# Performance work log

Hardware: AMD Instinct MI355X
Metric: run time of the kernel (lower is better)

Reference implementation:

```python
import jax, jax.numpy as jnp
import numpy as np

N = 50000   # nodes
E = 800000  # edges (avg degree 16)
D = 128     # node feature dim
DE = 16     # edge feature dim
H = 128     # MLP hidden dim
MSG_IN = 2 * D + DE + 1  # src feat + dst feat + edge feat + squared distance


def setup_inputs() -> dict:
    key = jax.random.key(0)
    ks = jax.random.split(key, 10)
    def wmat(k, shp):
        return jax.random.normal(k, shp, jnp.float32) * 0.05
    return {
        "f": jax.random.normal(ks[0], (N, D), jnp.float32),
        "x": jax.random.normal(ks[1], (N, 3), jnp.float32),
        "w": jax.random.normal(ks[2], (E, DE), jnp.float32),
        "src": jax.random.randint(ks[3], (E,), 0, N),
        "dst": jax.random.randint(ks[4], (E,), 0, N),
        "Wm1": wmat(ks[5], (MSG_IN, H)), "bm1": jnp.zeros((H,), jnp.float32),
        "Wm2": wmat(ks[6], (H, D)),      "bm2": jnp.zeros((D,), jnp.float32),
        "Wu1": wmat(ks[7], (D, H)),      "bu1": jnp.zeros((H,), jnp.float32),
        "Wu2": wmat(ks[8], (H, D)),      "bu2": jnp.zeros((D,), jnp.float32),
    }


def reference(f, x, w, src, dst, Wm1, bm1, Wm2, bm2, Wu1, bu1, Wu2, bu2):
    # message: gather endpoint features, squared distance, concat, MLP  [E, D]
    sqd = jnp.sum((x[src] - x[dst]) ** 2, axis=-1, keepdims=True)  # [E, 1]
    msg_in = jnp.concatenate([f[src], f[dst], w, sqd], axis=-1)    # [E, MSG_IN]
    m = jnp.dot(jax.nn.relu(jnp.dot(msg_in, Wm1) + bm1), Wm2) + bm2  # [E, D]
    # reduce: sum messages at destination nodes (DGL fn.sum)
    m_sum = jax.ops.segment_sum(m, dst, num_segments=N)             # [N, D]
    # update: node MLP on m_sum + f
    h = m_sum + f
    f_new = jnp.dot(jax.nn.relu(jnp.dot(h, Wu1) + bu1), Wu2) + bu2  # [N, D]
    return f_new
```

## Files before the change

kernel.cpp:

```cpp
#include <hip/hip_runtime.h>
#include <hip/hip_fp8.h>

#define D 128
#define HD 128
#define DE 16
#define MSG_IN 273
#define EB 64
#define NT 256
#define KP1 288
#define NCH2 4
#define NB 32
#define HID_PAD 132
#define CH8 (4 * EB * 64)
#define LDS1 (4 * EB * 64 + EB * 32)
#define OB 8192
#define OC 24576

typedef __attribute__((ext_vector_type(8))) short short8v;
typedef __attribute__((ext_vector_type(4))) float f32x4;
typedef unsigned short ushort_t;
typedef unsigned char uchar_t;

#define GLOAD_LDS16(gp, lp) \
    __builtin_amdgcn_global_load_lds((const __attribute__((address_space(1))) unsigned int*)(gp), \
                                     (__attribute__((address_space(3))) unsigned int*)(lp), 16, 0, 0)

__device__ __forceinline__ unsigned short f2bf(float v) {
    unsigned int u = __builtin_bit_cast(unsigned int, v);
    u += 0x7fffu + ((u >> 16) & 1u);
    return (unsigned short)(u >> 16);
}
__device__ __forceinline__ float bf2f(ushort_t u) {
    return __builtin_bit_cast(float, (unsigned int)u << 16);
}
__device__ __forceinline__ unsigned int cvt_pk_bf16(float lo, float hi) {
    unsigned int r;
    asm("v_cvt_pk_bf16_f32 %0, %1, %2" : "=v"(r) : "v"(lo), "v"(hi));
    return r;
}
__device__ __forceinline__ uchar_t f8e(float v) {
    __hip_fp8_e4m3 t(v);
    return (uchar_t)t.__x;
}
__device__ __forceinline__ float f8d(unsigned b) {
    unsigned t = ((b & 0x7fu) << 20) | ((b & 0x80u) << 24);
    return __builtin_bit_cast(float, t) * 0x1p120f;
}

__global__ void fused_pre_kernel(const float* __restrict__ Wm1, const float* __restrict__ Wm2,
                                 const float* __restrict__ Wu1, const float* __restrict__ Wu2,
                                 ushort_t* __restrict__ W1p, ushort_t* __restrict__ W2p,
                                 ushort_t* __restrict__ Wu1p, ushort_t* __restrict__ Wu2p,
                                 const float* __restrict__ f, ushort_t* __restrict__ fb,
                                 const float* __restrict__ w, ushort_t* __restrict__ wbf,
                                 const int* __restrict__ dst, int* __restrict__ cnt,
                                 int n8, int nw8, int E) {
    const int gid    = blockIdx.x * 256 + threadIdx.x;
    const int stride = gridDim.x * 256;
    const int rp1 = 128 * KP1;
    const int rp2 = rp1 + HD * D;
    const int rp_elems = rp2 + 2 * HD * D;
    for (int i = gid; i < rp_elems; i += stride) {
        if (i < rp1) {
            int n = i / KP1, k = i % KP1;
            W1p[i] = f2bf((k < MSG_IN) ? Wm1[(size_t)k * HD + n] : 0.f);
        } else if (i < rp2) {
            int i2 = i - rp1;
            int n = i2 / HD, k = i2 % HD;
            W2p[i2] = f2bf(Wm2[(size_t)k * D + n]);
        } else {
            int i2 = (i - rp2);
            const bool second = i2 >= HD * D;
            if (second) i2 -= HD * D;
            int n = i2 / HD, k = i2 % HD;
            if (second) Wu2p[i2] = f2bf(Wu2[(size_t)k * D + n]);
            else        Wu1p[i2] = f2bf(Wu1[(size_t)k * HD + n]);
        }
    }
    for (int i = gid; i < n8; i += stride) {
        float4 v0 = *(const float4*)(f + (size_t)i * 8);
        float4 v1 = *(const float4*)(f + (size_t)i * 8 + 4);
        union { ushort_t us[8]; short8v v; } pk;
        pk.us[0] = f2bf(v0.x); pk.us[1] = f2bf(v0.y);
        pk.us[2] = f2bf(v0.z); pk.us[3] = f2bf(v0.w);
        pk.us[4] = f2bf(v1.x); pk.us[5] = f2bf(v1.y);
        pk.us[6] = f2bf(v1.z); pk.us[7] = f2bf(v1.w);
        *(short8v*)(fb + (size_t)i * 8) = pk.v;
    }
    for (int i = gid; i < nw8; i += stride) {
        float4 v0 = *(const float4*)(w + (size_t)i * 8);
        float4 v1 = *(const float4*)(w + (size_t)i * 8 + 4);
        union { ushort_t us[8]; short8v v; } pk;
        pk.us[0] = f2bf(v0.x); pk.us[1] = f2bf(v0.y);
        pk.us[2] = f2bf(v0.z); pk.us[3] = f2bf(v0.w);
        pk.us[4] = f2bf(v1.x); pk.us[5] = f2bf(v1.y);
        pk.us[6] = f2bf(v1.z); pk.us[7] = f2bf(v1.w);
        *(short8v*)(wbf + (size_t)i * 8) = pk.v;
    }
    for (int i = gid; i < E; i += stride) atomicAdd(&cnt[dst[i]], 1);
}

__global__ __launch_bounds__(1024) void scan_kernel(const int* __restrict__ cnt,
                                                    int* __restrict__ roff,
                                                    int* __restrict__ cursor, int Nn) {
    __shared__ int wsum[16];
    const int t = threadIdx.x, l = t & 63, wid = t >> 6;
    int running = 0;
    for (int base = 0; base < Nn; base += 4096) {
        const int i0 = base + t * 4;
        int v0 = 0, v1 = 0, v2 = 0, v3 = 0;
        if (i0 + 3 < Nn) {
            int4 v = *(const int4*)(cnt + i0);
            v0 = v.x; v1 = v.y; v2 = v.z; v3 = v.w;
        } else {
            if (i0 + 0 < Nn) v0 = cnt[i0 + 0];
            if (i0 + 1 < Nn) v1 = cnt[i0 + 1];
            if (i0 + 2 < Nn) v2 = cnt[i0 + 2];
        }
        const int vsum = v0 + v1 + v2 + v3;
        int s = vsum;
        #pragma unroll
        for (int off = 1; off < 64; off <<= 1) {
            int u = __shfl_up(s, off, 64);
            if (l >= off) s += u;
        }
        if (l == 63) wsum[wid] = s;
        __syncthreads();
        if (wid == 0 && l < 16) {
            int xv = wsum[l];
            #pragma unroll
            for (int off = 1; off < 16; off <<= 1) {
                int u = __shfl_up(xv, off, 64);
                if (l >= off) xv += u;
            }
            wsum[l] = xv;
        }
        __syncthreads();
        const int prev  = (wid > 0) ? wsum[wid - 1] : 0;
        const int total = wsum[15];
        int ex = running + prev + (s - vsum);
        if (i0 + 0 < Nn) { roff[i0 + 0] = ex; cursor[i0 + 0] = ex; } ex += v0;
        if (i0 + 1 < Nn) { roff[i0 + 1] = ex; cursor[i0 + 1] = ex; } ex += v1;
        if (i0 + 2 < Nn) { roff[i0 + 2] = ex; cursor[i0 + 2] = ex; } ex += v2;
        if (i0 + 3 < Nn) { roff[i0 + 3] = ex; cursor[i0 + 3] = ex; }
        running += total;
        __syncthreads();
    }
}

__global__ void scatter_kernel(const int* __restrict__ dst, int* cursor,
                               const int* __restrict__ roff, const int* __restrict__ cnt,
                               int* __restrict__ perm, int* __restrict__ sdst,
                               float* __restrict__ mh, int E, int Nn) {
    const int gid    = blockIdx.x * 256 + threadIdx.x;
    const int stride = gridDim.x * 256;
    for (int i = gid; i < E; i += stride) {
        int d = dst[i];
        int s = atomicAdd(&cursor[d], 1);
        perm[s] = i;
        sdst[s] = d;
    }
    for (int n = gid; n < Nn; n += stride) {
        const int c = cnt[n];
        const int r = roff[n];
        const bool need0 = (c == 0) || (r / EB != (r + c - 1) / EB);
        if (need0) {
            float4 z = {0.f, 0.f, 0.f, 0.f};
            float* p = mh + (size_t)n * D;
            #pragma unroll
            for (int k = 0; k < 32; ++k) *(float4*)(p + k * 4) = z;
        }
    }
}

__global__ __launch_bounds__(NT, 4) void ab_kernel(
    const ushort_t* __restrict__ fbf,
    const ushort_t* __restrict__ W1p,
    uchar_t* __restrict__ Af, ushort_t* __restrict__ Bf16, int Nn)
{
    __shared__ __align__(16) ushort_t lds[2 * 64 * 64];

    const int t    = threadIdx.x;
    const int lane = t & 63;
    const int wv   = t >> 6;
    const int col  = lane & 15;
    const int g    = lane >> 4;
    const int n0   = blockIdx.x * 64;

    #pragma unroll
    for (int it = 0; it < 4; ++it) {
        const int gidx = it * 256 + t;
        const int row  = gidx >> 4;
        const int gr   = gidx & 15;
        const int pair = gr >> 3, s = gr & 7;
        const int sP   = s ^ (row & 7);
        const int gn   = min(n0 + row, Nn - 1);
        short8v v = *(const short8v*)(fbf + (size_t)gn * D + gr * 8);
        *(short8v*)&lds[(pair * 64 + row) * 64 + sP * 8] = v;
    }
    __syncthreads();

    const bool even = (col & 1) == 0;
    #pragma unroll
    for (int half = 0; half < 2; ++half) {
        f32x4 acc[4][2];
        #pragma unroll
        for (int rt = 0; rt < 4; ++rt) {
            acc[rt][0] = (f32x4){0.f, 0.f, 0.f, 0.f};
            acc[rt][1] = (f32x4){0.f, 0.f, 0.f, 0.f};
        }
        const int kbase = half * 128;
        #pragma unroll
        for (int c = 0; c < 4; ++c) {
            short8v b0 = *(const short8v*)&W1p[(size_t)(wv * 32 + col) * KP1 + kbase + c * 32 + g * 8];
            short8v b1 = *(const short8v*)&W1p[(size_t)(wv * 32 + 16 + col) * KP1 + kbase + c * 32 + g * 8];
            short8v a[4];
            #pragma unroll
            for (int rt = 0; rt < 4; ++rt) {
                const int row = rt * 16 + col;
                const int sP = (((c & 1) << 2) + g) ^ (row & 7);
                a[rt] = *(const short8v*)&lds[((c >> 1) * 64 + row) * 64 + sP * 8];
            }
            #pragma unroll
            for (int rt = 0; rt < 4; ++rt) {
                acc[rt][0] = __builtin_amdgcn_mfma_f32_16x16x32_bf16(a[rt], b0, acc[rt][0], 0, 0, 0);
                acc[rt][1] = __builtin_amdgcn_mfma_f32_16x16x32_bf16(a[rt], b1, acc[rt][1], 0, 0, 0);
            }
        }
        #pragma unroll
        for (int rt = 0; rt < 4; ++rt)
            #pragma unroll
            for (int j = 0; j < 2; ++j)
                #pragma unroll
                for (int r = 0; r < 4; ++r) {
                    const int row = rt * 16 + g * 4 + r;
                    const int gn = n0 + row;
                    float v  = acc[rt][j][r];
                    float vn = __shfl_xor(v, 1, 64);
                    if (even && gn < Nn) {
                        const int ca = wv * 32 + j * 16 + col;
                        if (half == 0) {
                            ushort_t pk = (ushort_t)f8e(v) | ((ushort_t)f8e(vn) << 8);
                            *(ushort_t*)(Af + (size_t)gn * D + ca) = pk;
                        } else {
                            *(unsigned int*)(Bf16 + (size_t)gn * D + ca) = cvt_pk_bf16(v, vn);
                        }
                    }
                }
    }
}

__global__ __launch_bounds__(NT, 4) void edge_lin_kernel(
    const uchar_t* __restrict__ Af, const ushort_t* __restrict__ Bf16,
    const float* __restrict__ x, const ushort_t* __restrict__ wbf,
    const int* __restrict__ src,
    const int* __restrict__ perm, const int* __restrict__ sdst,
    const ushort_t* __restrict__ W1p, const float* __restrict__ bm1,
    float* __restrict__ mh, int E)
{
    __shared__ __align__(16) uchar_t lds8[28672];
    __shared__ int s_rid[EB];
    __shared__ int s_dgs[EB];

    const int t    = threadIdx.x;
    const int lane = t & 63;
    const int wv   = t >> 6;
    const int e0   = blockIdx.x * EB;
    const int nvalid = min(EB, E - e0);

    const int myd  = (e0 + lane < E) ? sdst[e0 + lane] : -1;
    const int prevd = (e0 > 0) ? sdst[e0 - 1] : -2;
    const int nextd = (e0 + EB < E) ? sdst[e0 + EB] : -2;

    const int dprev_l = __shfl_up(myd, 1, 64);
    const bool head = (lane == 0) || (myd != dprev_l);
    const unsigned long long mask = __ballot(head && (lane < nvalid));
    const unsigned long long le = (lane == 63) ? ~0ull : ((1ull << (lane + 1)) - 1ull);
    const int rid = (int)__popcll(mask & le) - 1;
    const int ndist = (int)__popcll(mask);
    s_rid[lane] = (rid < 0) ? 0 : rid;
    if (head && lane < nvalid) s_dgs[rid] = myd;

    {
        const int el8 = lane >> 3;
        const int s   = lane & 7;
        const int sl  = s ^ el8;
        const int slA = min(e0 + wv * 16 + el8,     E - 1);
        const int slB = min(e0 + wv * 16 + 8 + el8, E - 1);
        const int nsA = src[perm[slA]];
        const int nsB = src[perm[slB]];
        GLOAD_LDS16(Af + (size_t)nsA * D + sl * 16, &lds8[(wv * 16    ) * 128]);
        GLOAD_LDS16(Af + (size_t)nsB * D + sl * 16, &lds8[(wv * 16 + 8) * 128]);
    }
    {
        const int ntask = ndist * 16;
        for (int idx = t; idx < ntask; idx += NT) {
            const int rowr = idx >> 4;
            const int gr   = idx & 15;
            const int dg   = s_dgs[rowr];
            uint4 v = *(const uint4*)(Bf16 + (size_t)dg * D + gr * 8);
            const int phys = gr ^ (rowr & 15);
            *(uint4*)&lds8[OB + rowr * 256 + phys * 16] = v;
        }
    }
    {
        const int el = lane >> 2, q = lane & 3;
        const int qp = q ^ (el & 3);
        const int slot = e0 + wv * 16 + el;
        const bool ok = slot < E;
        const int sc = min(slot, E - 1);
        const int ge = perm[sc];
        union { ushort_t us[8]; short8v v; } pk;
        #pragma unroll
        for (int j = 0; j < 8; ++j) pk.us[j] = 0;
        if (ok) {
            if (q < 2) {
                pk.v = *(const short8v*)(wbf + (size_t)ge * DE + q * 8);
            } else if (q == 2) {
                const int ns = src[ge], nd = sdst[sc];
                float dx = x[ns*3+0] - x[nd*3+0];
                float dy = x[ns*3+1] - x[nd*3+1];
                float dz = x[ns*3+2] - x[nd*3+2];
                pk.us[0] = f2bf(dx*dx + dy*dy + dz*dz);
            }
        }
        *(short8v*)&lds8[OC + (wv * 16 + el) * 64 + qp * 16] = pk.v;
    }

    const int col = lane & 15;
    const int g   = lane >> 4;

    short8v bc0 = *(const short8v*)&W1p[(size_t)(wv * 32 + col) * KP1 + 256 + g * 8];
    short8v bc1 = *(const short8v*)&W1p[(size_t)(wv * 32 + 16 + col) * KP1 + 256 + g * 8];

    __syncthreads();

    f32x4 acc[4][2];
    {
        float bv0 = bm1[wv * 32 + col];
        float bv1 = bm1[wv * 32 + 16 + col];
        #pragma unroll
        for (int rt = 0; rt < 4; ++rt) {
            acc[rt][0] = (f32x4){bv0, bv0, bv0, bv0};
            acc[rt][1] = (f32x4){bv1, bv1, bv1, bv1};
        }
    }
    #pragma unroll
    for (int rt = 0; rt < 4; ++rt) {
        const int row = rt * 16 + col;
        const int sP8 = g ^ (row & 3);
        short8v a = *(const short8v*)&lds8[OC + row * 64 + sP8 * 16];
        acc[rt][0] = __builtin_amdgcn_mfma_f32_16x16x32_bf16(a, bc0, acc[rt][0], 0, 0, 0);
        acc[rt][1] = __builtin_amdgcn_mfma_f32_16x16x32_bf16(a, bc1, acc[rt][1], 0, 0, 0);
    }

    float h[4][2][4];
    #pragma unroll
    for (int rt = 0; rt < 4; ++rt) {
        #pragma unroll
        for (int r = 0; r < 4; ++r) {
            const int row = rt * 16 + g * 4 + r;
            const int rd  = s_rid[row];
            #pragma unroll
            for (int j = 0; j < 2; ++j) {
                const int ca = wv * 32 + j * 16 + col;
                const uchar_t ab = lds8[row * 128 + (((ca >> 4) ^ (row & 7)) << 4) + (ca & 15)];
                const ushort_t bb = *(const ushort_t*)&lds8[OB + rd * 256 + (((ca >> 3) ^ (rd & 15)) << 4) + (ca & 7) * 2];
                h[rt][j][r] = fmaxf(acc[rt][j][r] + f8d(ab) + bf2f(bb), 0.f);
            }
        }
    }

    float qs[4][2];
    #pragma unroll
    for (int rt = 0; rt < 4; ++rt) {
        qs[rt][0] = (h[rt][0][0] + h[rt][0][1]) + (h[rt][0][2] + h[rt][0][3]);
        qs[rt][1] = (h[rt][1][0] + h[rt][1][1]) + (h[rt][1][2] + h[rt][1][3]);
    }
    unsigned long long rem = mask;
    while (rem) {
        const int beg = (int)__builtin_ctzll(rem);
        rem &= rem - 1;
        const int end = rem ? (int)__builtin_ctzll(rem) : nvalid;
        const int dg  = __shfl(myd, beg, 64);

        float s0 = 0.f, s1 = 0.f;
        #pragma unroll
        for (int rt = 0; rt < 4; ++rt) {
            const int qb = rt * 16 + g * 4;
            const int lo = max(qb, beg);
            const int hi = min(qb + 4, end);
            if (lo < hi) {
                if (lo == qb && hi == qb + 4) {
                    s0 += qs[rt][0]; s1 += qs[rt][1];
                } else {
                    #pragma unroll
                    for (int r = 0; r < 4; ++r) {
                        const int sl = qb + r;
                        if (sl >= beg && sl < end) {
                            s0 += h[rt][0][r]; s1 += h[rt][1][r];
                        }
                    }
                }
            }
        }
        s0 += __shfl_xor(s0, 16, 64); s0 += __shfl_xor(s0, 32, 64);
        s1 += __shfl_xor(s1, 16, 64); s1 += __shfl_xor(s1, 32, 64);
        if (g == 0) {
            const bool bnd = (beg == 0 && dg == prevd) || (end == nvalid && dg == nextd);
            float* p = mh + (size_t)dg * D + wv * 32 + col;
            if (bnd) { atomicAdd(p, s0); atomicAdd(p + 16, s1); }
            else     { p[0] = s0; p[16] = s1; }
        }
    }
}

__global__ __launch_bounds__(NT, 4) void mh2msum_kernel(
    const float* __restrict__ mh, const int* __restrict__ cnt,
    const ushort_t* __restrict__ W2p, const float* __restrict__ bm2,
    float* __restrict__ msum, int Nn)
{
    __shared__ __align__(16) ushort_t lds[2 * 64 * 64];
    __shared__ int s_cnt[64];

    const int t    = threadIdx.x;
    const int lane = t & 63;
    const int wv   = t >> 6;
    const int col  = lane & 15;
    const int g    = lane >> 4;
    const int n0   = blockIdx.x * 64;

    if (t < 64) s_cnt[t] = (n0 + t < Nn) ? cnt[n0 + t] : 0;

    #pragma unroll
    for (int it = 0; it < 4; ++it) {
        const int gidx = it * 256 + t;
        const int row  = gidx >> 4;
        const int gr   = gidx & 15;
        const int pair = gr >> 3, s = gr & 7;
        const int sP   = s ^ (row & 7);
        const int gn   = n0 + row;
        union { ushort_t us[8]; short8v v; } pk;
        if (gn < Nn) {
            const size_t off = (size_t)gn * D + gr * 8;
            float4 m0 = *(const float4*)(mh + off);
            float4 m1 = *(const float4*)(mh + off + 4);
            pk.us[0] = f2bf(m0.x); pk.us[1] = f2bf(m0.y);
            pk.us[2] = f2bf(m0.z); pk.us[3] = f2bf(m0.w);
            pk.us[4] = f2bf(m1.x); pk.us[5] = f2bf(m1.y);
            pk.us[6] = f2bf(m1.z); pk.us[7] = f2bf(m1.w);
        } else {
            #pragma unroll
            for (int j = 0; j < 8; ++j) pk.us[j] = 0;
        }
        *(short8v*)&lds[(pair * 64 + row) * 64 + sP * 8] = pk.v;
    }
    __syncthreads();

    f32x4 acc[4][2];
    {
        const float bv0 = bm2[wv * 32 + col];
        const float bv1 = bm2[wv * 32 + 16 + col];
        #pragma unroll
        for (int rt = 0; rt < 4; ++rt)
            #pragma unroll
            for (int r = 0; r < 4; ++r) {
                const float cn = (float)s_cnt[rt * 16 + g * 4 + r];
                acc[rt][0][r] = cn * bv0;
                acc[rt][1][r] = cn * bv1;
            }
    }
    #pragma unroll
    for (int c = 0; c < 4; ++c) {
        short8v b0 = *(const short8v*)&W2p[(size_t)(wv * 32 + col) * HD + c * 32 + g * 8];
        short8v b1 = *(const short8v*)&W2p[(size_t)(wv * 32 + 16 + col) * HD + c * 32 + g * 8];
        short8v a[4];
        #pragma unroll
        for (int rt = 0; rt < 4; ++rt) {
            const int row = rt * 16 + col;
            const int sP = (((c & 1) << 2) + g) ^ (row & 7);
            a[rt] = *(const short8v*)&lds[((c >> 1) * 64 + row) * 64 + sP * 8];
        }
        #pragma unroll
        for (int rt = 0; rt < 4; ++rt) {
            acc[rt][0] = __builtin_amdgcn_mfma_f32_16x16x32_bf16(a[rt], b0, acc[rt][0], 0, 0, 0);
            acc[rt][1] = __builtin_amdgcn_mfma_f32_16x16x32_bf16(a[rt], b1, acc[rt][1], 0, 0, 0);
        }
    }

    #pragma unroll
    for (int rt = 0; rt < 4; ++rt)
        #pragma unroll
        for (int r = 0; r < 4; ++r) {
            const int row = rt * 16 + g * 4 + r;
            const int gn = n0 + row;
            if (gn < Nn) {
                msum[(size_t)gn * D + wv * 32 + col]      = acc[rt][0][r];
                msum[(size_t)gn * D + wv * 32 + 16 + col] = acc[rt][1][r];
            }
        }
}

__global__ __launch_bounds__(NT, 4) void node_mfma_kernel(
    const float* __restrict__ f, const float* __restrict__ msum,
    const ushort_t* __restrict__ Wu1p, const float* __restrict__ bu1,
    const ushort_t* __restrict__ Wu2p, const float* __restrict__ bu2,
    float* __restrict__ out, int Nn)
{
    __shared__ __align__(16) ushort_t lds[2 * 64 * 64];

    const int t    = threadIdx.x;
    const int lane = t & 63;
    const int wv   = t >> 6;
    const int col  = lane & 15;
    const int g    = lane >> 4;
    const int n0   = blockIdx.x * 64;

    #pragma unroll
    for (int it = 0; it < 4; ++it) {
        const int gidx = it * 256 + t;
        const int row  = gidx >> 4;
        const int gr   = gidx & 15;
        const int pair = gr >> 3, s = gr & 7;
        const int sP   = s ^ (row & 7);
        const int gn   = n0 + row;
        union { ushort_t us[8]; short8v v; } pk;
        if (gn < Nn) {
            const size_t off = (size_t)gn * D + gr * 8;
            float4 m0 = *(const float4*)(msum + off);
            float4 m1 = *(const float4*)(msum + off + 4);
            float4 f0 = *(const float4*)(f + off);
            float4 f1 = *(const float4*)(f + off + 4);
            pk.us[0] = f2bf(m0.x + f0.x); pk.us[1] = f2bf(m0.y + f0.y);
            pk.us[2] = f2bf(m0.z + f0.z); pk.us[3] = f2bf(m0.w + f0.w);
            pk.us[4] = f2bf(m1.x + f1.x); pk.us[5] = f2bf(m1.y + f1.y);
            pk.us[6] = f2bf(m1.z + f1.z); pk.us[7] = f2bf(m1.w + f1.w);
        } else {
            #pragma unroll
            for (int j = 0; j < 8; ++j) pk.us[j] = 0;
        }
        *(short8v*)&lds[(pair * 64 + row) * 64 + sP * 8] = pk.v;
    }

    const size_t wrow0 = (size_t)(wv * 32 + col) * HD;
    const size_t wrow1 = (size_t)(wv * 32 + 16 + col) * HD;
    short8v nb0 = *(const short8v*)&Wu1p[wrow0 + g * 8];
    short8v nb1 = *(const short8v*)&Wu1p[wrow1 + g * 8];

    __syncthreads();

    f32x4 acc[4][2];
    {
        float bv0 = bu1[wv * 32 + col];
        float bv1 = bu1[wv * 32 + 16 + col];
        #pragma unroll
        for (int rt = 0; rt < 4; ++rt) {
            acc[rt][0] = (f32x4){bv0, bv0, bv0, bv0};
            acc[rt][1] = (f32x4){bv1, bv1, bv1, bv1};
        }
    }
    #pragma unroll
    for (int c = 0; c < 4; ++c) {
        short8v b0 = nb0, b1 = nb1;
        if (c + 1 < 4) {
            nb0 = *(const short8v*)&Wu1p[wrow0 + (c + 1) * 32 + g * 8];
            nb1 = *(const short8v*)&Wu1p[wrow1 + (c + 1) * 32 + g * 8];
        }
        short8v a[4];
        #pragma unroll
        for (int rt = 0; rt < 4; ++rt) {
            const int row = rt * 16 + col;
            const int sP = (((c & 1) << 2) + g) ^ (row & 7);
            a[rt] = *(const short8v*)&lds[((c >> 1) * 64 + row) * 64 + sP * 8];
        }
        #pragma unroll
        for (int rt = 0; rt < 4; ++rt) {
            acc[rt][0] = __builtin_amdgcn_mfma_f32_16x16x32_bf16(a[rt], b0, acc[rt][0], 0, 0, 0);
            acc[rt][1] = __builtin_amdgcn_mfma_f32_16x16x32_bf16(a[rt], b1, acc[rt][1], 0, 0, 0);
        }
    }
    __syncthreads();

    const int ph = wv >> 1;
    #pragma unroll
    for (int rt = 0; rt < 4; ++rt)
        #pragma unroll
        for (int j = 0; j < 2; ++j)
            #pragma unroll
            for (int r = 0; r < 4; ++r) {
                const int row = rt * 16 + g * 4 + r;
                float v = fmaxf(acc[rt][j][r], 0.f);
                unsigned int pk2 = cvt_pk_bf16(v, v);
                const int sH = (((wv & 1) << 2) + j * 2 + (col >> 3)) ^ (row & 7);
                lds[(ph * 64 + row) * 64 + sH * 8 + (col & 7)] = (ushort_t)pk2;
            }
    __syncthreads();

    const size_t w2r0 = (size_t)(wv * 32 + col) * HD;
    const size_t w2r1 = (size_t)(wv * 32 + 16 + col) * HD;
    short8v m0 = *(const short8v*)&Wu2p[w2r0 + g * 8];
    short8v m1 = *(const short8v*)&Wu2p[w2r1 + g * 8];
    f32x4 acc2[4][2];
    {
        float bv0 = bu2[wv * 32 + col];
        float bv1 = bu2[wv * 32 + 16 + col];
        #pragma unroll
        for (int rt = 0; rt < 4; ++rt) {
            acc2[rt][0] = (f32x4){bv0, bv0, bv0, bv0};
            acc2[rt][1] = (f32x4){bv1, bv1, bv1, bv1};
        }
    }
    #pragma unroll
    for (int c = 0; c < 4; ++c) {
        short8v b0 = m0, b1 = m1;
        if (c + 1 < 4) {
            m0 = *(const short8v*)&Wu2p[w2r0 + (c + 1) * 32 + g * 8];
            m1 = *(const short8v*)&Wu2p[w2r1 + (c + 1) * 32 + g * 8];
        }
        short8v a[4];
        #pragma unroll
        for (int rt = 0; rt < 4; ++rt) {
            const int row = rt * 16 + col;
            const int sP = (((c & 1) << 2) + g) ^ (row & 7);
            a[rt] = *(const short8v*)&lds[((c >> 1) * 64 + row) * 64 + sP * 8];
        }
        #pragma unroll
        for (int rt = 0; rt < 4; ++rt) {
            acc2[rt][0] = __builtin_amdgcn_mfma_f32_16x16x32_bf16(a[rt], b0, acc2[rt][0], 0, 0, 0);
            acc2[rt][1] = __builtin_amdgcn_mfma_f32_16x16x32_bf16(a[rt], b1, acc2[rt][1], 0, 0, 0);
        }
    }

    #pragma unroll
    for (int rt = 0; rt < 4; ++rt)
        #pragma unroll
        for (int r = 0; r < 4; ++r) {
            const int row = rt * 16 + g * 4 + r;
            const int gn = n0 + row;
            if (gn < Nn) {
                out[(size_t)gn * D + wv * 32 + col]      = acc2[rt][0][r];
                out[(size_t)gn * D + wv * 32 + 16 + col] = acc2[rt][1][r];
            }
        }
}


__global__ void repack_kernel(const float* __restrict__ Wm1, const float* __restrict__ Wm2,
                              ushort_t* __restrict__ W1p, ushort_t* __restrict__ W2p) {
    int idx = blockIdx.x * 256 + threadIdx.x;
    const int n1 = 128 * KP1;
    if (idx < n1) {
        int n = idx / KP1, k = idx % KP1;
        W1p[idx] = f2bf((k < MSG_IN) ? Wm1[(size_t)k * HD + n] : 0.f);
    } else {
        int i2 = idx - n1;
        if (i2 < HD * D) {
            int n = i2 / HD, k = i2 % HD;
            W2p[i2] = f2bf(Wm2[(size_t)k * D + n]);
        }
    }
}

__global__ void fconv_kernel(const float* __restrict__ f, ushort_t* __restrict__ fb, int n8) {
    int i = blockIdx.x * 256 + threadIdx.x;
    if (i < n8) {
        float4 v0 = *(const float4*)(f + (size_t)i * 8);
        float4 v1 = *(const float4*)(f + (size_t)i * 8 + 4);
        union { ushort_t us[8]; short8v v; } pk;
        pk.us[0] = f2bf(v0.x); pk.us[1] = f2bf(v0.y);
        pk.us[2] = f2bf(v0.z); pk.us[3] = f2bf(v0.w);
        pk.us[4] = f2bf(v1.x); pk.us[5] = f2bf(v1.y);
        pk.us[6] = f2bf(v1.z); pk.us[7] = f2bf(v1.w);
        *(short8v*)(fb + (size_t)i * 8) = pk.v;
    }
}

__global__ __launch_bounds__(NT, 4) void edge_mfma_kernel(
    const ushort_t* __restrict__ fbf, const float* __restrict__ x,
    const float* __restrict__ w, const int* __restrict__ src,
    const int* __restrict__ dst,
    const ushort_t* __restrict__ W1p, const float* __restrict__ bm1,
    const ushort_t* __restrict__ W2p, const float* __restrict__ bm2,
    ushort_t* msum, int E)
{
    __shared__ __align__(16) ushort_t lds[LDS1];
    __shared__ int s_dst[EB];

    const int t    = threadIdx.x;
    const int lane = t & 63;
    const int wv   = t >> 6;
    const int e0   = blockIdx.x * EB;

    if (t < EB) s_dst[t] = (e0 + t < E) ? dst[e0 + t] : 0;
    {
        const int el8 = lane >> 3;
        const int s   = lane & 7;
        const int sl  = s ^ el8;
        const int geA = min(e0 + wv * 16 + el8,     E - 1);
        const int geB = min(e0 + wv * 16 + 8 + el8, E - 1);
        const int nsA = src[geA], ndA = dst[geA];
        const int nsB = src[geB], ndB = dst[geB];
        #pragma unroll
        for (int p = 0; p < 4; ++p) {
            const int n0 = (p < 2) ? nsA : ndA;
            const int n1 = (p < 2) ? nsB : ndB;
            const ushort_t* g0 = fbf + (size_t)n0 * D + (p & 1) * 64 + sl * 8;
            const ushort_t* g1 = fbf + (size_t)n1 * D + (p & 1) * 64 + sl * 8;
            GLOAD_LDS16(g0, &lds[(p * EB + wv * 16    ) * 64]);
            GLOAD_LDS16(g1, &lds[(p * EB + wv * 16 + 8) * 64]);
        }
    }
    {
        const int el = lane >> 2, q = lane & 3;
        const int qp = q ^ (el & 3);
        const int ge = e0 + wv * 16 + el;
        const bool ok = ge < E;
        const int gc = min(ge, E - 1);
        union { ushort_t us[8]; short8v v; } pk;
        #pragma unroll
        for (int j = 0; j < 8; ++j) pk.us[j] = 0;
        if (ok) {
            if (q < 2) {
                float4 w0 = *(const float4*)(w + (size_t)gc * DE + q * 8);
                float4 w1 = *(const float4*)(w + (size_t)gc * DE + q * 8 + 4);
                pk.us[0] = f2bf(w0.x); pk.us[1] = f2bf(w0.y);
                pk.us[2] = f2bf(w0.z); pk.us[3] = f2bf(w0.w);
                pk.us[4] = f2bf(w1.x); pk.us[5] = f2bf(w1.y);
                pk.us[6] = f2bf(w1.z); pk.us[7] = f2bf(w1.w);
            } else if (q == 2) {
                const int ns = src[gc], nd = dst[gc];
                float dx = x[ns*3+0] - x[nd*3+0];
                float dy = x[ns*3+1] - x[nd*3+1];
                float dz = x[ns*3+2] - x[nd*3+2];
                pk.us[0] = f2bf(dx*dx + dy*dy + dz*dz);
            }
        }
        *(short8v*)&lds[CH8 + (wv * 16 + el) * 32 + qp * 8] = pk.v;
    }

    const int col = lane & 15;
    const int g   = lane >> 4;
    const size_t wrow0 = (size_t)(wv * 32 + col) * KP1;
    const size_t wrow1 = (size_t)(wv * 32 + 16 + col) * KP1;
    short8v nb0 = *(const short8v*)&W1p[wrow0 + g * 8];
    short8v nb1 = *(const short8v*)&W1p[wrow1 + g * 8];
    __syncthreads();

    f32x4 acc[4][2];
    {
        float bv0 = bm1[wv * 32 + col];
        float bv1 = bm1[wv * 32 + 16 + col];
        #pragma unroll
        for (int rt = 0; rt < 4; ++rt) {
            acc[rt][0] = (f32x4){bv0, bv0, bv0, bv0};
            acc[rt][1] = (f32x4){bv1, bv1, bv1, bv1};
        }
    }
    #pragma unroll
    for (int c = 0; c < 9; ++c) {
        short8v b0 = nb0, b1 = nb1;
        if (c + 1 < 9) {
            nb0 = *(const short8v*)&W1p[wrow0 + (c + 1) * 32 + g * 8];
            nb1 = *(const short8v*)&W1p[wrow1 + (c + 1) * 32 + g * 8];
        }
        short8v a[4];
        #pragma unroll
        for (int rt = 0; rt < 4; ++rt) {
            const int row = rt * 16 + col;
            if (c < 8) {
                const int sP = (((c & 1) << 2) + g) ^ (row & 7);
                a[rt] = *(const short8v*)&lds[((c >> 1) * EB + row) * 64 + sP * 8];
            } else {
                const int sP = g ^ (row & 3);
                a[rt] = *(const short8v*)&lds[CH8 + row * 32 + sP * 8];
            }
        }
        #pragma unroll
        for (int rt = 0; rt < 4; ++rt) {
            acc[rt][0] = __builtin_amdgcn_mfma_f32_16x16x32_bf16(a[rt], b0, acc[rt][0], 0, 0, 0);
            acc[rt][1] = __builtin_amdgcn_mfma_f32_16x16x32_bf16(a[rt], b1, acc[rt][1], 0, 0, 0);
        }
    }
    __syncthreads();

    const int ph = wv >> 1;
    #pragma unroll
    for (int rt = 0; rt < 4; ++rt)
        #pragma unroll
        for (int j = 0; j < 2; ++j)
            #pragma unroll
            for (int r = 0; r < 4; ++r) {
                const int row = rt * 16 + g * 4 + r;
                float v = fmaxf(acc[rt][j][r], 0.f);
                unsigned int pk2 = cvt_pk_bf16(v, v);
                const int sH = (((wv & 1) << 2) + j * 2 + (col >> 3)) ^ (row & 7);
                lds[(ph * EB + row) * 64 + sH * 8 + (col & 7)] = (ushort_t)pk2;
            }
    __syncthreads();

    const size_t w2r0 = (size_t)(wv * 32 + col) * HD;
    const size_t w2r1 = (size_t)(wv * 32 + 16 + col) * HD;
    short8v m0 = *(const short8v*)&W2p[w2r0 + g * 8];
    short8v m1 = *(const short8v*)&W2p[w2r1 + g * 8];
    f32x4 acc2[4][2];
    {
        float bv0 = bm2[wv * 32 + col];
        float bv1 = bm2[wv * 32 + 16 + col];
        #pragma unroll
        for (int rt = 0; rt < 4; ++rt) {
            acc2[rt][0] = (f32x4){bv0, bv0, bv0, bv0};
            acc2[rt][1] = (f32x4){bv1, bv1, bv1, bv1};
        }
    }
    #pragma unroll
    for (int c = 0; c < NCH2; ++c) {
        short8v b0 = m0, b1 = m1;
        if (c + 1 < NCH2) {
            m0 = *(const short8v*)&W2p[w2r0 + (c + 1) * 32 + g * 8];
            m1 = *(const short8v*)&W2p[w2r1 + (c + 1) * 32 + g * 8];
        }
        short8v a[4];
        #pragma unroll
        for (int rt = 0; rt < 4; ++rt) {
            const int row = rt * 16 + col;
            const int sP = (((c & 1) << 2) + g) ^ (row & 7);
            a[rt] = *(const short8v*)&lds[((c >> 1) * EB + row) * 64 + sP * 8];
        }
        #pragma unroll
        for (int rt = 0; rt < 4; ++rt) {
            acc2[rt][0] = __builtin_amdgcn_mfma_f32_16x16x32_bf16(a[rt], b0, acc2[rt][0], 0, 0, 0);
            acc2[rt][1] = __builtin_amdgcn_mfma_f32_16x16x32_bf16(a[rt], b1, acc2[rt][1], 0, 0, 0);
        }
    }

    const bool even = (col & 1) == 0;
    #pragma unroll
    for (int rt = 0; rt < 4; ++rt)
        #pragma unroll
        for (int r = 0; r < 4; ++r) {
            const int e  = rt * 16 + g * 4 + r;
            const int ge = e0 + e;
            const int dg = s_dst[e];
            #pragma unroll
            for (int j = 0; j < 2; ++j) {
                float v  = acc2[rt][j][r];
                float vn = __shfl_xor(v, 1, 64);
                if (even && ge < E) {
                    unsigned int pk2 = cvt_pk_bf16(v, vn);
                    ushort_t* p = msum + (size_t)dg * D + wv * 32 + j * 16 + col;
                    asm volatile("global_atomic_pk_add_bf16 %0, %1, off"
                                 :: "v"(p), "v"(pk2) : "memory");
                }
            }
        }
}

template<bool MB16>
__global__ __launch_bounds__(NT, 4) void node_kernel(
    const float* __restrict__ f, const void* __restrict__ msum_v,
    const float* __restrict__ Wu1, const float* __restrict__ bu1,
    const float* __restrict__ Wu2, const float* __restrict__ bu2,
    float* out, int Nn)
{
    __shared__ __align__(16) float hin[NB][HID_PAD];
    __shared__ __align__(16) float hid[NB][HID_PAD];
    const int t  = threadIdx.x;
    const int n0 = blockIdx.x * NB;
    const int nn = min(NB, Nn - n0);

    {
        #pragma unroll
        for (int it = 0; it < 4; ++it) {
            const int idx = it * 1024 + t * 4;
            const int e   = idx >> 7;
            const int cb  = idx & 127;
            if (e < nn) {
                const size_t off = (size_t)(n0 + e) * D + cb;
                float4 mv;
                if (MB16) {
                    uint2 pk = *(const uint2*)((const ushort_t*)msum_v + off);
                    mv.x = bf2f((ushort_t)(pk.x & 0xffffu));
                    mv.y = bf2f((ushort_t)(pk.x >> 16));
                    mv.z = bf2f((ushort_t)(pk.y & 0xffffu));
                    mv.w = bf2f((ushort_t)(pk.y >> 16));
                } else {
                    mv = *(const float4*)((const float*)msum_v + off);
                }
                float4 fv = *(const float4*)&f[off];
                float4 o = {mv.x + fv.x, mv.y + fv.y, mv.z + fv.z, mv.w + fv.w};
                *(float4*)&hin[e][cb] = o;
            }
        }
    }
    __syncthreads();

    const int tc = t & 15, te2 = (t >> 4) * 2, c0 = tc * 8;
    float a1[2][8];
    #pragma unroll
    for (int c = 0; c < 8; ++c) { float bv = bu1[c0 + c]; a1[0][c] = bv; a1[1][c] = bv; }
    for (int i = 0; i < D; i += 4) {
        float m0[4], m1[4];
        *(float4*)m0 = *(const float4*)&hin[te2][i];
        *(float4*)m1 = *(const float4*)&hin[te2 + 1][i];
        #pragma unroll
        for (int r = 0; r < 4; ++r) {
            float wr[8];
            *(float4*)&wr[0] = *(const float4*)(Wu1 + (size_t)(i + r) * HD + c0);
            *(float4*)&wr[4] = *(const float4*)(Wu1 + (size_t)(i + r) * HD + c0 + 4);
            #pragma unroll
            for (int c = 0; c < 8; ++c) { a1[0][c] += m0[r]*wr[c]; a1[1][c] += m1[r]*wr[c]; }
        }
    }
    #pragma unroll
    for (int j = 0; j < 2; ++j) {
        float v[8];
        #pragma unroll
        for (int c = 0; c < 8; ++c) v[c] = fmaxf(a1[j][c], 0.f);
        *(float4*)&hid[te2 + j][c0] = *(float4*)&v[0];
        *(float4*)&hid[te2 + j][c0 + 4] = *(float4*)&v[4];
    }
    __syncthreads();
    float a2[2][8];
    #pragma unroll
    for (int c = 0; c < 8; ++c) { float bv = bu2[c0 + c]; a2[0][c] = bv; a2[1][c] = bv; }
    for (int h = 0; h < HD; h += 4) {
        float m0[4], m1[4];
        *(float4*)m0 = *(const float4*)&hid[te2][h];
        *(float4*)m1 = *(const float4*)&hid[te2 + 1][h];
        #pragma unroll
        for (int r = 0; r < 4; ++r) {
            float wr[8];
            *(float4*)&wr[0] = *(const float4*)(Wu2 + (size_t)(h + r) * D + c0);
            *(float4*)&wr[4] = *(const float4*)(Wu2 + (size_t)(h + r) * D + c0 + 4);
            #pragma unroll
            for (int c = 0; c < 8; ++c) { a2[0][c] += m0[r]*wr[c]; a2[1][c] += m1[r]*wr[c]; }
        }
    }
    #pragma unroll
    for (int j = 0; j < 2; ++j) {
        int e = te2 + j, gn = n0 + e;
        if (e < nn) {
            *(float4*)(out + (size_t)gn * D + c0) = *(float4*)&a2[j][0];
            *(float4*)(out + (size_t)gn * D + c0 + 4) = *(float4*)&a2[j][4];
        }
    }
}

extern "C" void kernel_launch(void* const* d_in, const int* in_sizes, int n_in,
                              void* d_out, int out_size, void* d_ws, size_t ws_size,
                              hipStream_t stream) {
    const float* f   = (const float*)d_in[0];
    const float* x   = (const float*)d_in[1];
    const float* w   = (const float*)d_in[2];
    const int*   src = (const int*)d_in[3];
    const int*   dst = (const int*)d_in[4];
    const float* Wm1 = (const float*)d_in[5];
    const float* bm1 = (const float*)d_in[6];
    const float* Wm2 = (const float*)d_in[7];
    const float* bm2 = (const float*)d_in[8];
    const float* Wu1 = (const float*)d_in[9];
    const float* bu1 = (const float*)d_in[10];
    const float* Wu2 = (const float*)d_in[11];
    const float* bu2 = (const float*)d_in[12];

    const int Nn = in_sizes[0] / D;
    const int E  = in_sizes[3];

    const size_t wbytes  = (size_t)(128 * KP1 + HD * D) * sizeof(ushort_t);
    const size_t wubytes = (size_t)(2 * HD * D) * sizeof(ushort_t);
    auto align512 = [](size_t v) { return (v + 511) & ~(size_t)511; };
    char* wsb = (char*)d_ws;

    size_t off = 0;
    const size_t o_w    = off; off = align512(off + wbytes);
    const size_t o_wu   = off; off = align512(off + wubytes);
    const size_t o_fb   = off; off = align512(off + (size_t)Nn * D * 2);
    const size_t o_wbf  = off; off = align512(off + (size_t)E * DE * 2);
    const size_t o_af   = off; off = align512(off + (size_t)Nn * D);
    const size_t o_bf16 = off; off = align512(off + (size_t)Nn * D * 2);
    const size_t o_cnt  = off; off = align512(off + (size_t)Nn * 4);
    const size_t o_roff = off; off = align512(off + (size_t)Nn * 4);
    const size_t o_cur  = off; off = align512(off + (size_t)Nn * 4);
    const size_t o_perm = off; off = align512(off + (size_t)E * 4);
    const size_t o_sdst = off; off = align512(off + (size_t)E * 4);
    const size_t o_mh   = off; off = align512(off + (size_t)Nn * D * 4);
    const size_t o_ms   = off; off = align512(off + (size_t)Nn * D * 4);
    const size_t primary_total = off;

    if (ws_size >= primary_total) {
        ushort_t* W1p  = (ushort_t*)(wsb + o_w);
        ushort_t* W2p  = W1p + 128 * KP1;
        ushort_t* Wu1p = (ushort_t*)(wsb + o_wu);
        ushort_t* Wu2p = Wu1p + HD * D;
        ushort_t* fbf  = (ushort_t*)(wsb + o_fb);
        ushort_t* wbf  = (ushort_t*)(wsb + o_wbf);
        uchar_t*  Af   = (uchar_t*)(wsb + o_af);
        ushort_t* Bf16 = (ushort_t*)(wsb + o_bf16);
        int* cnt       = (int*)(wsb + o_cnt);
        int* roff      = (int*)(wsb + o_roff);
        int* cursor    = (int*)(wsb + o_cur);
        int* perm      = (int*)(wsb + o_perm);
        int* sdst      = (int*)(wsb + o_sdst);
        float* mh      = (float*)(wsb + o_mh);
        float* msum    = (float*)(wsb + o_ms);

        const int n8  = Nn * D / 8;
        const int nw8 = E * DE / 8;
        const int ntiles = (E + EB - 1) / EB;
        const int nblk   = (Nn + 63) / 64;
        hipMemsetAsync(cnt, 0, (size_t)Nn * 4, stream);
        fused_pre_kernel<<<dim3(1024), dim3(256), 0, stream>>>(
            Wm1, Wm2, Wu1, Wu2, W1p, W2p, Wu1p, Wu2p, f, fbf, w, wbf, dst, cnt, n8, nw8, E);
        scan_kernel<<<dim3(1), dim3(1024), 0, stream>>>(cnt, roff, cursor, Nn);
        scatter_kernel<<<dim3((E + 255) / 256), dim3(256), 0, stream>>>(
            dst, cursor, roff, cnt, perm, sdst, mh, E, Nn);
        ab_kernel<<<dim3(nblk), dim3(NT), 0, stream>>>(fbf, W1p, Af, Bf16, Nn);
        edge_lin_kernel<<<dim3(ntiles), dim3(NT), 0, stream>>>(
            Af, Bf16, x, wbf, src, perm, sdst, W1p, bm1, mh, E);
        mh2msum_kernel<<<dim3(nblk), dim3(NT), 0, stream>>>(mh, cnt, W2p, bm2, msum, Nn);
        node_mfma_kernel<<<dim3(nblk), dim3(NT), 0, stream>>>(
            f, msum, Wu1p, bu1, Wu2p, bu2, (float*)d_out, Nn);
        return;
    }

    size_t off2 = 0;
    const size_t p_w  = off2; off2 = align512(off2 + wbytes);
    const size_t p_fb = off2; off2 = align512(off2 + (size_t)Nn * D * 2);
    const size_t p_ms = off2; off2 = align512(off2 + (size_t)Nn * D * 2);
    if (ws_size >= off2) {
        ushort_t* W1p  = (ushort_t*)(wsb + p_w);
        ushort_t* W2p  = W1p + 128 * KP1;
        ushort_t* fbf  = (ushort_t*)(wsb + p_fb);
        ushort_t* msum = (ushort_t*)(wsb + p_ms);
        const int rp_elems = 128 * KP1 + HD * D;
        hipMemsetAsync(msum, 0, (size_t)Nn * D * 2, stream);
        repack_kernel<<<dim3((rp_elems + 255) / 256), dim3(256), 0, stream>>>(Wm1, Wm2, W1p, W2p);
        const int n8 = Nn * D / 8;
        fconv_kernel<<<dim3((n8 + 255) / 256), dim3(256), 0, stream>>>(f, fbf, n8);
        edge_mfma_kernel<<<dim3((E + EB - 1) / EB), dim3(NT), 0, stream>>>(
            fbf, x, w, src, dst, W1p, bm1, W2p, bm2, msum, E);
        node_kernel<true><<<dim3((Nn + NB - 1) / NB), dim3(NT), 0, stream>>>(
            f, msum, Wu1, bu1, Wu2, bu2, (float*)d_out, Nn);
        return;
    }
}
```

Baseline: 267.9 us.

## Fuse node-side msum and update MLP kernels; convert f to bf16 inside ab_kernel

The f→bf16 conversion moves out of the pre-kernel and into ab_kernel, which now reads fp32 f directly and packs it into LDS. This removes the bf16 copy of f and its write/read round trip. mh2msum and node_mfma are merged into one node_fused_kernel: the msum tile stays in registers, gets f added, and is written to LDS as bf16 for the update MLP. That drops the fp32 msum buffer and one launch. The cost is one longer kernel with more register pressure, and the software prefetch of Wu1/Wu2 weights is gone.

```diff
diff --git a/kernel.cpp b/kernel.cpp
--- a/kernel.cpp
+++ b/kernel.cpp
@@ -51,10 +51,9 @@
                                  const float* __restrict__ Wu1, const float* __restrict__ Wu2,
                                  ushort_t* __restrict__ W1p, ushort_t* __restrict__ W2p,
                                  ushort_t* __restrict__ Wu1p, ushort_t* __restrict__ Wu2p,
-                                 const float* __restrict__ f, ushort_t* __restrict__ fb,
                                  const float* __restrict__ w, ushort_t* __restrict__ wbf,
                                  const int* __restrict__ dst, int* __restrict__ cnt,
-                                 int n8, int nw8, int E) {
+                                 int nw8, int E) {
     const int gid    = blockIdx.x * 256 + threadIdx.x;
     const int stride = gridDim.x * 256;
     const int rp1 = 128 * KP1;
@@ -77,16 +76,6 @@
             else        Wu1p[i2] = f2bf(Wu1[(size_t)k * HD + n]);
         }
     }
-    for (int i = gid; i < n8; i += stride) {
-        float4 v0 = *(const float4*)(f + (size_t)i * 8);
-        float4 v1 = *(const float4*)(f + (size_t)i * 8 + 4);
-        union { ushort_t us[8]; short8v v; } pk;
-        pk.us[0] = f2bf(v0.x); pk.us[1] = f2bf(v0.y);
-        pk.us[2] = f2bf(v0.z); pk.us[3] = f2bf(v0.w);
-        pk.us[4] = f2bf(v1.x); pk.us[5] = f2bf(v1.y);
-        pk.us[6] = f2bf(v1.z); pk.us[7] = f2bf(v1.w);
-        *(short8v*)(fb + (size_t)i * 8) = pk.v;
-    }
     for (int i = gid; i < nw8; i += stride) {
         float4 v0 = *(const float4*)(w + (size_t)i * 8);
         float4 v1 = *(const float4*)(w + (size_t)i * 8 + 4);
@@ -174,7 +163,7 @@
 }
 
 __global__ __launch_bounds__(NT, 4) void ab_kernel(
-    const ushort_t* __restrict__ fbf,
+    const float* __restrict__ f,
     const ushort_t* __restrict__ W1p,
     uchar_t* __restrict__ Af, ushort_t* __restrict__ Bf16, int Nn)
 {
@@ -195,8 +184,15 @@
         const int pair = gr >> 3, s = gr & 7;
         const int sP   = s ^ (row & 7);
         const int gn   = min(n0 + row, Nn - 1);
-        short8v v = *(const short8v*)(fbf + (size_t)gn * D + gr * 8);
-        *(short8v*)&lds[(pair * 64 + row) * 64 + sP * 8] = v;
+        const size_t off = (size_t)gn * D + gr * 8;
+        float4 v0 = *(const float4*)(f + off);
+        float4 v1 = *(const float4*)(f + off + 4);
+        union { ushort_t us[8]; short8v v; } pk;
+        pk.us[0] = f2bf(v0.x); pk.us[1] = f2bf(v0.y);
+        pk.us[2] = f2bf(v0.z); pk.us[3] = f2bf(v0.w);
+        pk.us[4] = f2bf(v1.x); pk.us[5] = f2bf(v1.y);
+        pk.us[6] = f2bf(v1.z); pk.us[7] = f2bf(v1.w);
+        *(short8v*)&lds[(pair * 64 + row) * 64 + sP * 8] = pk.v;
     }
     __syncthreads();
 
@@ -415,10 +411,13 @@
     }
 }
 
-__global__ __launch_bounds__(NT, 4) void mh2msum_kernel(
-    const float* __restrict__ mh, const int* __restrict__ cnt,
+__global__ __launch_bounds__(NT, 4) void node_fused_kernel(
+    const float* __restrict__ f, const float* __restrict__ mh,
+    const int* __restrict__ cnt,
     const ushort_t* __restrict__ W2p, const float* __restrict__ bm2,
-    float* __restrict__ msum, int Nn)
+    const ushort_t* __restrict__ Wu1p, const float* __restrict__ bu1,
+    const ushort_t* __restrict__ Wu2p, const float* __restrict__ bu2,
+    float* __restrict__ out, int Nn)
 {
     __shared__ __align__(16) ushort_t lds[2 * 64 * 64];
     __shared__ int s_cnt[64];
@@ -487,85 +486,43 @@
             acc[rt][1] = __builtin_amdgcn_mfma_f32_16x16x32_bf16(a[rt], b1, acc[rt][1], 0, 0, 0);
         }
     }
-
+    __syncthreads();
+
+    const int ph = wv >> 1;
     #pragma unroll
     for (int rt = 0; rt < 4; ++rt)
         #pragma unroll
         for (int r = 0; r < 4; ++r) {
             const int row = rt * 16 + g * 4 + r;
             const int gn = n0 + row;
-            if (gn < Nn) {
-                msum[(size_t)gn * D + wv * 32 + col]      = acc[rt][0][r];
-                msum[(size_t)gn * D + wv * 32 + 16 + col] = acc[rt][1][r];
-            }
-        }
-}
-
-__global__ __launch_bounds__(NT, 4) void node_mfma_kernel(
-    const float* __restrict__ f, const float* __restrict__ msum,
-    const ushort_t* __restrict__ Wu1p, const float* __restrict__ bu1,
-    const ushort_t* __restrict__ Wu2p, const float* __restrict__ bu2,
-    float* __restrict__ out, int Nn)
-{
-    __shared__ __align__(16) ushort_t lds[2 * 64 * 64];
-
-    const int t    = threadIdx.x;
-    const int lane = t & 63;
-    const int wv   = t >> 6;
-    const int col  = lane & 15;
-    const int g    = lane >> 4;
-    const int n0   = blockIdx.x * 64;
-
-    #pragma unroll
-    for (int it = 0; it < 4; ++it) {
-        const int gidx = it * 256 + t;
-        const int row  = gidx >> 4;
-        const int gr   = gidx & 15;
-        const int pair = gr >> 3, s = gr & 7;
-        const int sP   = s ^ (row & 7);
-        const int gn   = n0 + row;
-        union { ushort_t us[8]; short8v v; } pk;
-        if (gn < Nn) {
-            const size_t off = (size_t)gn * D + gr * 8;
-            float4 m0 = *(const float4*)(msum + off);
-            float4 m1 = *(const float4*)(msum + off + 4);
-            float4 f0 = *(const float4*)(f + off);
-            float4 f1 = *(const float4*)(f + off + 4);
-            pk.us[0] = f2bf(m0.x + f0.x); pk.us[1] = f2bf(m0.y + f0.y);
-            pk.us[2] = f2bf(m0.z + f0.z); pk.us[3] = f2bf(m0.w + f0.w);
-            pk.us[4] = f2bf(m1.x + f1.x); pk.us[5] = f2bf(m1.y + f1.y);
-            pk.us[6] = f2bf(m1.z + f1.z); pk.us[7] = f2bf(m1.w + f1.w);
-        } else {
-            #pragma unroll
-            for (int j = 0; j < 8; ++j) pk.us[j] = 0;
-        }
-        *(short8v*)&lds[(pair * 64 + row) * 64 + sP * 8] = pk.v;
-    }
+            #pragma unroll
+            for (int j = 0; j < 2; ++j) {
+                const int ca = wv * 32 + j * 16 + col;
+                float v = 0.f;
+                if (gn < Nn) v = acc[rt][j][r] + f[(size_t)gn * D + ca];
+                unsigned int pk2 = cvt_pk_bf16(v, v);
+                const int sH = (((wv & 1) << 2) + j * 2 + (col >> 3)) ^ (row & 7);
+                lds[(ph * 64 + row) * 64 + sH * 8 + (col & 7)] = (ushort_t)pk2;
+            }
+        }
+    __syncthreads();
 
     const size_t wrow0 = (size_t)(wv * 32 + col) * HD;
     const size_t wrow1 = (size_t)(wv * 32 + 16 + col) * HD;
-    short8v nb0 = *(const short8v*)&Wu1p[wrow0 + g * 8];
-    short8v nb1 = *(const short8v*)&Wu1p[wrow1 + g * 8];
-
-    __syncthreads();
-
-    f32x4 acc[4][2];
+    f32x4 acc1[4][2];
     {
         float bv0 = bu1[wv * 32 + col];
         float bv1 = bu1[wv * 32 + 16 + col];
         #pragma unroll
         for (int rt = 0; rt < 4; ++rt) {
-            acc[rt][0] = (f32x4){bv0, bv0, bv0, bv0};
-            acc[rt][1] = (f32x4){bv1, bv1, bv1, bv1};
+            acc1[rt][0] = (f32x4){bv0, bv0, bv0, bv0};
+            acc1[rt][1] = (f32x4){bv1, bv1, bv1, bv1};
         }
     }
     #pragma unroll
     for (int c = 0; c < 4; ++c) {
-        short8v b0 = nb0, b1 = nb1;
-        if (c + 1 < 4) {
-            nb0 = *(const short8v*)&Wu1p[wrow0 + (c + 1) * 32 + g * 8];
-            nb1 = *(const short8v*)&Wu1p[wrow1 + (c + 1) * 32 + g * 8];
-        }
+        short8v b0 = *(const short8v*)&Wu1p[wrow0 + c * 32 + g * 8];
+        short8v b1 = *(const short8v*)&Wu1p[wrow1 + c * 32 + g * 8];
         short8v a[4];
         #pragma unroll
         for (int rt = 0; rt < 4; ++rt) {
@@ -575,13 +532,12 @@
         }
         #pragma unroll
         for (int rt = 0; rt < 4; ++rt) {
-            acc[rt][0] = __builtin_amdgcn_mfma_f32_16x16x32_bf16(a[rt], b0, acc[rt][0], 0, 0, 0);
-            acc[rt][1] = __builtin_amdgcn_mfma_f32_16x16x32_bf16(a[rt], b1, acc[rt][1], 0, 0, 0);
-        }
-    }
-    __syncthreads();
-
-    const int ph = wv >> 1;
+            acc1[rt][0] = __builtin_amdgcn_mfma_f32_16x16x32_bf16(a[rt], b0, acc1[rt][0], 0, 0, 0);
+            acc1[rt][1] = __builtin_amdgcn_mfma_f32_16x16x32_bf16(a[rt], b1, acc1[rt][1], 0, 0, 0);
+        }
+    }
+    __syncthreads();
+
     #pragma unroll
     for (int rt = 0; rt < 4; ++rt)
         #pragma unroll
@@ -589,17 +545,13 @@
             #pragma unroll
             for (int r = 0; r < 4; ++r) {
                 const int row = rt * 16 + g * 4 + r;
-                float v = fmaxf(acc[rt][j][r], 0.f);
+                float v = fmaxf(acc1[rt][j][r], 0.f);
                 unsigned int pk2 = cvt_pk_bf16(v, v);
                 const int sH = (((wv & 1) << 2) + j * 2 + (col >> 3)) ^ (row & 7);
                 lds[(ph * 64 + row) * 64 + sH * 8 + (col & 7)] = (ushort_t)pk2;
             }
     __syncthreads();
 
-    const size_t w2r0 = (size_t)(wv * 32 + col) * HD;
-    const size_t w2r1 = (size_t)(wv * 32 + 16 + col) * HD;
-    short8v m0 = *(const short8v*)&Wu2p[w2r0 + g * 8];
-    short8v m1 = *(const short8v*)&Wu2p[w2r1 + g * 8];
     f32x4 acc2[4][2];
     {
         float bv0 = bu2[wv * 32 + col];
@@ -612,11 +564,8 @@
     }
     #pragma unroll
     for (int c = 0; c < 4; ++c) {
-        short8v b0 = m0, b1 = m1;
-        if (c + 1 < 4) {
-            m0 = *(const short8v*)&Wu2p[w2r0 + (c + 1) * 32 + g * 8];
-            m1 = *(const short8v*)&Wu2p[w2r1 + (c + 1) * 32 + g * 8];
-        }
+        short8v b0 = *(const short8v*)&Wu2p[wrow0 + c * 32 + g * 8];
+        short8v b1 = *(const short8v*)&Wu2p[wrow1 + c * 32 + g * 8];
         short8v a[4];
         #pragma unroll
         for (int rt = 0; rt < 4; ++rt) {
@@ -974,7 +923,6 @@
     size_t off = 0;
     const size_t o_w    = off; off = align512(off + wbytes);
     const size_t o_wu   = off; off = align512(off + wubytes);
-    const size_t o_fb   = off; off = align512(off + (size_t)Nn * D * 2);
     const size_t o_wbf  = off; off = align512(off + (size_t)E * DE * 2);
     const size_t o_af   = off; off = align512(off + (size_t)Nn * D);
     const size_t o_bf16 = off; off = align512(off + (size_t)Nn * D * 2);
@@ -984,7 +932,6 @@
     const size_t o_perm = off; off = align512(off + (size_t)E * 4);
     const size_t o_sdst = off; off = align512(off + (size_t)E * 4);
     const size_t o_mh   = off; off = align512(off + (size_t)Nn * D * 4);
-    const size_t o_ms   = off; off = align512(off + (size_t)Nn * D * 4);
     const size_t primary_total = off;
 
     if (ws_size >= primary_total) {
@@ -992,7 +939,6 @@
         ushort_t* W2p  = W1p + 128 * KP1;
         ushort_t* Wu1p = (ushort_t*)(wsb + o_wu);
         ushort_t* Wu2p = Wu1p + HD * D;
-        ushort_t* fbf  = (ushort_t*)(wsb + o_fb);
         ushort_t* wbf  = (ushort_t*)(wsb + o_wbf);
         uchar_t*  Af   = (uchar_t*)(wsb + o_af);
         ushort_t* Bf16 = (ushort_t*)(wsb + o_bf16);
@@ -1002,24 +948,21 @@
         int* perm      = (int*)(wsb + o_perm);
         int* sdst      = (int*)(wsb + o_sdst);
         float* mh      = (float*)(wsb + o_mh);
-        float* msum    = (float*)(wsb + o_ms);
-
-        const int n8  = Nn * D / 8;
+
         const int nw8 = E * DE / 8;
         const int ntiles = (E + EB - 1) / EB;
         const int nblk   = (Nn + 63) / 64;
         hipMemsetAsync(cnt, 0, (size_t)Nn * 4, stream);
         fused_pre_kernel<<<dim3(1024), dim3(256), 0, stream>>>(
-            Wm1, Wm2, Wu1, Wu2, W1p, W2p, Wu1p, Wu2p, f, fbf, w, wbf, dst, cnt, n8, nw8, E);
+            Wm1, Wm2, Wu1, Wu2, W1p, W2p, Wu1p, Wu2p, w, wbf, dst, cnt, nw8, E);
         scan_kernel<<<dim3(1), dim3(1024), 0, stream>>>(cnt, roff, cursor, Nn);
         scatter_kernel<<<dim3((E + 255) / 256), dim3(256), 0, stream>>>(
             dst, cursor, roff, cnt, perm, sdst, mh, E, Nn);
-        ab_kernel<<<dim3(nblk), dim3(NT), 0, stream>>>(fbf, W1p, Af, Bf16, Nn);
+        ab_kernel<<<dim3(nblk), dim3(NT), 0, stream>>>(f, W1p, Af, Bf16, Nn);
         edge_lin_kernel<<<dim3(ntiles), dim3(NT), 0, stream>>>(
             Af, Bf16, x, wbf, src, perm, sdst, W1p, bm1, mh, E);
-        mh2msum_kernel<<<dim3(nblk), dim3(NT), 0, stream>>>(mh, cnt, W2p, bm2, msum, Nn);
-        node_mfma_kernel<<<dim3(nblk), dim3(NT), 0, stream>>>(
-            f, msum, Wu1p, bu1, Wu2p, bu2, (float*)d_out, Nn);
+        node_fused_kernel<<<dim3(nblk), dim3(NT), 0, stream>>>(
+            f, mh, cnt, W2p, bm2, Wu1p, bu1, Wu2p, bu2, (float*)d_out, Nn);
         return;
     }
 
```

Measured after the change: 261.0 us. 1.03x faster.
